# Performance work log

Hardware: AMD Instinct MI355X
Metric: run time of the kernel (lower is better)

## Reference

```python
import jax, jax.numpy as jnp
import numpy as np

EPS = 1e-6
LAM = 0.005


def setup_inputs() -> dict:
    key = jax.random.key(0)
    k1, k2, k3 = jax.random.split(key, 3)
    B, D, H, W, M = 16, 256, 128, 128, 4096
    z = jax.random.normal(k1, (B, D, H, W), dtype=jnp.float32)
    z_prime = jax.random.normal(k2, (B, D, H, W), dtype=jnp.float32)
    # Precomputed sampled pixel indices (flat over H*W). With randn inputs every
    # pixel passes the validity mask, so uniform sampling matches the original.
    flat_idx = jax.random.randint(k3, (B, M), 0, H * W, dtype=jnp.int32)
    return {"z": z, "z_prime": z_prime, "flat_idx": flat_idx}


def _gather_pixels(z, flat_idx):
    # z: (B, D, H, W), flat_idx: (B, M) -> (B*M, D)
    B, D, H, W = z.shape
    M = flat_idx.shape[1]
    z_flat = z.reshape(B, D, H * W)
    g = jnp.take_along_axis(z_flat, flat_idx[:, None, :], axis=2)  # (B, D, M)
    return g.transpose(0, 2, 1).reshape(B * M, D)


def _normalise(x):
    mean = jnp.mean(x, axis=0, keepdims=True)
    std = jnp.std(x, axis=0, keepdims=True, ddof=1)  # torch .std() is unbiased
    return (x - mean) / jnp.clip(std, EPS, None)


def reference(z, z_prime, flat_idx):
    D = z.shape[1]
    zm = _normalise(_gather_pixels(z, flat_idx))        # (N, D)
    zpm = _normalise(_gather_pixels(z_prime, flat_idx))  # (N, D)
    N = zm.shape[0]
    C = (zm.T @ zpm) / N                                 # (D, D)
    on_diag = jnp.diagonal(C)
    off_diag = C.reshape(-1)[1:].reshape(D - 1, D + 1)[:, :-1]
    loss = jnp.sum((1.0 - on_diag) ** 2) + LAM * jnp.sum(off_diag ** 2)
    return loss
```

## Files before the change

kernel.cpp:

```cpp
#include <hip/hip_runtime.h>
#include <hip/hip_bf16.h>

typedef short s16x8 __attribute__((ext_vector_type(8)));
typedef float f32x16 __attribute__((ext_vector_type(16)));

namespace {
constexpr int kB = 16;
constexpr int kD = 256;
constexpr int kHW = 16384;
constexpr int kM = 4096;
constexpr int kN = kB * kM;
constexpr int kWin = 1024;
constexpr int kNBlk = kB * (kHW / kWin);
constexpr int kKT = 32;
constexpr int kNIter = kWin / kKT;
constexpr float kLam = 0.005f;

__device__ __forceinline__ unsigned short f2bf(float f) {
    union { float f; unsigned u; } x{f};
    const unsigned r = x.u + 0x7FFFu + ((x.u >> 16) & 1u);
    return (unsigned short)(r >> 16);
}
}

__global__ __launch_bounds__(256) void count_kernel(
    const int* __restrict__ flat_idx, int* __restrict__ cnt)
{
    __shared__ int h[kHW];
    const int t = threadIdx.x;
    const int b = blockIdx.x;
    for (int i = t; i < kHW; i += 256) h[i] = 0;
    __syncthreads();
    const int* bi = flat_idx + b * kM;
    for (int i = t; i < kM; i += 256) atomicAdd(&h[bi[i]], 1);
    __syncthreads();
    int* dst = cnt + b * kHW;
    for (int i = t; i < kHW; i += 256) dst[i] = h[i];
}

__global__ __launch_bounds__(512, 2) void fused_gram_kernel(
    const float* __restrict__ z, const float* __restrict__ zp,
    const int* __restrict__ cnt,
    float* __restrict__ partial, float* __restrict__ statsPart)
{
    __shared__ char smem[65536];

    const int bx = blockIdx.x;
    const int b = bx & (kB - 1);
    const int win0 = (bx >> 4) * kWin;
    const int t = threadIdx.x;
    const int w = t >> 6, lane = t & 63, l31 = lane & 31, half = lane >> 5;
    const int wr = w >> 2;
    const int wc = w & 3;
    const int rbase = t >> 3;
    const int cg = t & 7;

    const float* zb  = z  + (size_t)b * kD * kHW;
    const float* zpb = zp + (size_t)b * kD * kHW;
    const int* cb = cnt + b * kHW;

    f32x16 acc[4][2];
#pragma unroll
    for (int i = 0; i < 4; ++i)
#pragma unroll
        for (int j = 0; j < 2; ++j)
#pragma unroll
            for (int r = 0; r < 16; ++r) acc[i][j][r] = 0.f;

    float sA[4], ssA[4], sB[4], ssB[4];
#pragma unroll
    for (int q = 0; q < 4; ++q) { sA[q] = ssA[q] = sB[q] = ssB[q] = 0.f; }

    float4 va[4], vb[4];
    int4 ci;

    auto LOAD = [&](int kt) {
        const int base = win0 + kt * kKT + cg * 4;
#pragma unroll
        for (int q = 0; q < 4; ++q) {
            const int row = 64 * q + rbase;
            va[q] = *(const float4*)(zb  + (size_t)row * kHW + base);
            vb[q] = *(const float4*)(zpb + (size_t)row * kHW + base);
        }
        ci = *(const int4*)(cb + base);
    };

    auto CONVERT = [&](int buf) {
        char* As = smem + buf * 32768;
        char* Bs = As + 16384;
        const float cf[4] = {(float)ci.x, (float)ci.y, (float)ci.z, (float)ci.w};
#pragma unroll
        for (int q = 0; q < 4; ++q) {
            const int row = 64 * q + rbase;
            const float a[4]  = {va[q].x, va[q].y, va[q].z, va[q].w};
            const float bb[4] = {vb[q].x, vb[q].y, vb[q].z, vb[q].w};
            ushort4 pa, pb;
            unsigned short* pav = (unsigned short*)&pa;
            unsigned short* pbv = (unsigned short*)&pb;
#pragma unroll
            for (int j = 0; j < 4; ++j) {
                const float wa = cf[j] * a[j];
                const float wb = cf[j] * bb[j];
                sA[q] += wa; ssA[q] += wa * a[j];
                sB[q] += wb; ssB[q] += wb * bb[j];
                pav[j] = f2bf(a[j]);
                pbv[j] = f2bf(wb);
            }
            const int off = row * 64 + (((cg >> 1) ^ ((row >> 1) & 3)) << 4)
                          + ((cg & 1) << 3);
            *(ushort4*)(As + off) = pa;
            *(ushort4*)(Bs + off) = pb;
        }
    };

    LOAD(0);
    CONVERT(0);
    LOAD(1);
    __syncthreads();

    for (int kt = 0; kt < kNIter; ++kt) {
        const char* As = smem + (kt & 1) * 32768;
        const char* Bs = As + 16384;
#pragma unroll
        for (int ks = 0; ks < 2; ++ks) {
            s16x8 af[4], bfr[2];
#pragma unroll
            for (int rt = 0; rt < 4; ++rt) {
                const int row = 128 * wr + 32 * rt + l31;
                const int o = (2 * ks + half) ^ ((row >> 1) & 3);
                af[rt] = *(const s16x8*)(As + row * 64 + o * 16);
            }
#pragma unroll
            for (int ct = 0; ct < 2; ++ct) {
                const int row = 64 * wc + 32 * ct + l31;
                const int o = (2 * ks + half) ^ ((row >> 1) & 3);
                bfr[ct] = *(const s16x8*)(Bs + row * 64 + o * 16);
            }
#pragma unroll
            for (int rt = 0; rt < 4; ++rt)
#pragma unroll
                for (int ct = 0; ct < 2; ++ct)
                    acc[rt][ct] = __builtin_amdgcn_mfma_f32_32x32x16_bf16(
                        af[rt], bfr[ct], acc[rt][ct], 0, 0, 0);
        }
        __syncthreads();
        if (kt < kNIter - 1) {
            CONVERT((kt + 1) & 1);
            if (kt < kNIter - 2) LOAD(kt + 2);
        }
        __syncthreads();
    }

    float* out = partial + (size_t)bx * (kD * kD);
#pragma unroll
    for (int rt = 0; rt < 4; ++rt)
#pragma unroll
        for (int ct = 0; ct < 2; ++ct)
#pragma unroll
            for (int r = 0; r < 16; ++r) {
                const int row = 128 * wr + 32 * rt + (r & 3) + 8 * (r >> 2) + 4 * half;
                const int col = 64 * wc + 32 * ct + l31;
                out[row * kD + col] = acc[rt][ct][r];
            }

    float* sd = (float*)smem;
#pragma unroll
    for (int q = 0; q < 4; ++q) {
        const int row = 64 * q + rbase;
        float* p = sd + (row * 8 + cg) * 4;
        p[0] = sA[q]; p[1] = ssA[q]; p[2] = sB[q]; p[3] = ssB[q];
    }
    __syncthreads();
    {
        const int row = t >> 1;
        const int pair = t & 1;
        float a0 = 0.f, a1 = 0.f;
#pragma unroll
        for (int g = 0; g < 8; ++g) {
            a0 += sd[(row * 8 + g) * 4 + 2 * pair];
            a1 += sd[(row * 8 + g) * 4 + 2 * pair + 1];
        }
        float* p = statsPart + ((size_t)bx * kD + row) * 4;
        p[2 * pair] = a0;
        p[2 * pair + 1] = a1;
    }
}

__global__ __launch_bounds__(256) void reduce_gram_kernel(
    const float* __restrict__ partial, float* __restrict__ G)
{
    const int d = blockIdx.x;
    const int e = threadIdx.x;
    float s = 0.f;
#pragma unroll 8
    for (int c = 0; c < kNBlk; ++c)
        s += partial[(size_t)c * (kD * kD) + d * kD + e];
    G[d * kD + e] = s;
}

__global__ __launch_bounds__(256) void loss_kernel(
    const float* __restrict__ G, const float* __restrict__ statsPart,
    float* __restrict__ out)
{
    __shared__ float muA[kD], isA[kD], muB[kD], isB[kD];
    const int t = threadIdx.x;
    float sA = 0.f, ssA = 0.f, sB = 0.f, ssB = 0.f;
    for (int blk = 0; blk < kNBlk; ++blk) {
        const float4 v = *(const float4*)(statsPart + ((size_t)blk * kD + t) * 4);
        sA += v.x; ssA += v.y; sB += v.z; ssB += v.w;
    }
    const float n = (float)kN;
    const float mA = sA / n, mB = sB / n;
    const float vA = (ssA - n * mA * mA) / (n - 1.f);
    const float vB = (ssB - n * mB * mB) / (n - 1.f);
    const float sdA = fmaxf(sqrtf(fmaxf(vA, 0.f)), 1e-6f);
    const float sdB = fmaxf(sqrtf(fmaxf(vB, 0.f)), 1e-6f);
    muA[t] = mA; isA[t] = 1.f / sdA;
    muB[t] = mB; isB[t] = 1.f / sdB;
    __syncthreads();

    float acc = 0.f;
    for (int d = 0; d < kD; ++d) {
        const int e = t;
        const float c = (G[d * kD + e] / n - muA[d] * muB[e]) * isA[d] * isB[e];
        if (d == e) { const float u = 1.f - c; acc += u * u; }
        else        { acc += kLam * c * c; }
    }
#pragma unroll
    for (int o = 32; o; o >>= 1) acc += __shfl_down(acc, o);
    __shared__ float r[4];
    if ((t & 63) == 0) r[t >> 6] = acc;
    __syncthreads();
    if (t == 0) out[0] = r[0] + r[1] + r[2] + r[3];
}

extern "C" void kernel_launch(void* const* d_in, const int* in_sizes, int n_in,
                              void* d_out, int out_size, void* d_ws, size_t ws_size,
                              hipStream_t stream) {
    const float* z  = (const float*)d_in[0];
    const float* zp = (const float*)d_in[1];
    const int* flat_idx = (const int*)d_in[2];
    float* out = (float*)d_out;

    char* ws = (char*)d_ws;
    int* cnt = (int*)ws;
    float* statsPart = (float*)(ws + (size_t)1 * 1024 * 1024);
    float* G = (float*)(ws + (size_t)2 * 1024 * 1024);
    float* partial = (float*)(ws + (size_t)16 * 1024 * 1024);

    count_kernel<<<kB, 256, 0, stream>>>(flat_idx, cnt);
    fused_gram_kernel<<<kNBlk, 512, 0, stream>>>(z, zp, cnt, partial, statsPart);
    reduce_gram_kernel<<<kD, 256, 0, stream>>>(partial, G);
    loss_kernel<<<1, 256, 0, stream>>>(G, statsPart, out);
}
```

Measured before the change: 182.1 us.

## Deepen gram-kernel prefetch to two register sets and parallelise stats reduction

The gram kernel now keeps two register sets of prefetched inputs, so global loads run two k-tiles ahead and the bf16 conversion of the next tile is issued before the MFMA step of the current one. The per-row statistics accumulation is rewritten as fma chains. The per-block statistics reduction, previously a serial 256-block loop inside the single-block loss kernel, moves into the reduce_gram kernel as a wave-shuffle reduction spread over all 256 blocks. The extra prefetch set raises register pressure under the 512x2 launch bound and could cause spills.

```diff
diff --git a/kernel.cpp b/kernel.cpp
--- a/kernel.cpp
+++ b/kernel.cpp
@@ -71,55 +71,56 @@
 #pragma unroll
     for (int q = 0; q < 4; ++q) { sA[q] = ssA[q] = sB[q] = ssB[q] = 0.f; }
 
-    float4 va[4], vb[4];
-    int4 ci;
-
-    auto LOAD = [&](int kt) {
-        const int base = win0 + kt * kKT + cg * 4;
-#pragma unroll
-        for (int q = 0; q < 4; ++q) {
-            const int row = 64 * q + rbase;
-            va[q] = *(const float4*)(zb  + (size_t)row * kHW + base);
-            vb[q] = *(const float4*)(zpb + (size_t)row * kHW + base);
-        }
-        ci = *(const int4*)(cb + base);
-    };
-
-    auto CONVERT = [&](int buf) {
-        char* As = smem + buf * 32768;
-        char* Bs = As + 16384;
-        const float cf[4] = {(float)ci.x, (float)ci.y, (float)ci.z, (float)ci.w};
-#pragma unroll
-        for (int q = 0; q < 4; ++q) {
-            const int row = 64 * q + rbase;
-            const float a[4]  = {va[q].x, va[q].y, va[q].z, va[q].w};
-            const float bb[4] = {vb[q].x, vb[q].y, vb[q].z, vb[q].w};
-            ushort4 pa, pb;
-            unsigned short* pav = (unsigned short*)&pa;
-            unsigned short* pbv = (unsigned short*)&pb;
-#pragma unroll
-            for (int j = 0; j < 4; ++j) {
-                const float wa = cf[j] * a[j];
-                const float wb = cf[j] * bb[j];
-                sA[q] += wa; ssA[q] += wa * a[j];
-                sB[q] += wb; ssB[q] += wb * bb[j];
-                pav[j] = f2bf(a[j]);
-                pbv[j] = f2bf(wb);
-            }
-            const int off = row * 64 + (((cg >> 1) ^ ((row >> 1) & 3)) << 4)
-                          + ((cg & 1) << 3);
-            *(ushort4*)(As + off) = pa;
-            *(ushort4*)(Bs + off) = pb;
-        }
-    };
-
-    LOAD(0);
-    CONVERT(0);
-    LOAD(1);
-    __syncthreads();
-
-    for (int kt = 0; kt < kNIter; ++kt) {
-        const char* As = smem + (kt & 1) * 32768;
+    float4 va0[4], vb0[4], va1[4], vb1[4];
+    int4 ci0, ci1;
+
+#define LOAD_SET(S, kt)                                                     \
+    {                                                                       \
+        const int base_ = win0 + (kt) * kKT + cg * 4;                       \
+        _Pragma("unroll")                                                   \
+        for (int q = 0; q < 4; ++q) {                                       \
+            const int row_ = 64 * q + rbase;                                \
+            va##S[q] = *(const float4*)(zb  + (size_t)row_ * kHW + base_);  \
+            vb##S[q] = *(const float4*)(zpb + (size_t)row_ * kHW + base_);  \
+        }                                                                   \
+        ci##S = *(const int4*)(cb + base_);                                 \
+    }
+
+#define CONV_SET(S, buf)                                                    \
+    {                                                                       \
+        char* As_ = smem + (buf) * 32768;                                   \
+        char* Bs_ = As_ + 16384;                                            \
+        const float cf_[4] = {(float)ci##S.x, (float)ci##S.y,               \
+                              (float)ci##S.z, (float)ci##S.w};              \
+        _Pragma("unroll")                                                   \
+        for (int q = 0; q < 4; ++q) {                                       \
+            const int row_ = 64 * q + rbase;                                \
+            const float a_[4]  = {va##S[q].x, va##S[q].y, va##S[q].z, va##S[q].w}; \
+            const float bb_[4] = {vb##S[q].x, vb##S[q].y, vb##S[q].z, vb##S[q].w}; \
+            ushort4 pa_, pb_;                                               \
+            unsigned short* pav_ = (unsigned short*)&pa_;                   \
+            unsigned short* pbv_ = (unsigned short*)&pb_;                   \
+            _Pragma("unroll")                                               \
+            for (int j = 0; j < 4; ++j) {                                   \
+                const float a2_ = a_[j] * a_[j];                            \
+                const float b2_ = bb_[j] * bb_[j];                          \
+                const float wb_ = cf_[j] * bb_[j];                          \
+                sA[q] = fmaf(cf_[j], a_[j], sA[q]);                         \
+                ssA[q] = fmaf(cf_[j], a2_, ssA[q]);                         \
+                sB[q] = fmaf(cf_[j], bb_[j], sB[q]);                        \
+                ssB[q] = fmaf(cf_[j], b2_, ssB[q]);                         \
+                pav_[j] = f2bf(a_[j]);                                      \
+                pbv_[j] = f2bf(wb_);                                        \
+            }                                                               \
+            const int off_ = row_ * 64 + (((cg >> 1) ^ ((row_ >> 1) & 3)) << 4) \
+                           + ((cg & 1) << 3);                               \
+            *(ushort4*)(As_ + off_) = pa_;                                  \
+            *(ushort4*)(Bs_ + off_) = pb_;                                  \
+        }                                                                   \
+    }
+
+    auto MFMA_STEP = [&](int buf) {
+        const char* As = smem + buf * 32768;
         const char* Bs = As + 16384;
 #pragma unroll
         for (int ks = 0; ks < 2; ++ks) {
@@ -143,11 +144,23 @@
                     acc[rt][ct] = __builtin_amdgcn_mfma_f32_32x32x16_bf16(
                         af[rt], bfr[ct], acc[rt][ct], 0, 0, 0);
         }
+    };
+
+    LOAD_SET(0, 0)
+    CONV_SET(0, 0)
+    LOAD_SET(1, 1)
+    LOAD_SET(0, 2)
+    __syncthreads();
+
+    for (int kt = 0; kt < kNIter; kt += 2) {
+        CONV_SET(1, 1)
+        if (kt + 3 < kNIter) LOAD_SET(1, kt + 3)
+        MFMA_STEP(0);
         __syncthreads();
-        if (kt < kNIter - 1) {
-            CONVERT((kt + 1) & 1);
-            if (kt < kNIter - 2) LOAD(kt + 2);
-        }
+
+        if (kt + 2 < kNIter) CONV_SET(0, 0)
+        if (kt + 4 < kNIter) LOAD_SET(0, kt + 4)
+        MFMA_STEP(1);
         __syncthreads();
     }
 
@@ -184,10 +197,13 @@
         p[2 * pair] = a0;
         p[2 * pair + 1] = a1;
     }
+#undef LOAD_SET
+#undef CONV_SET
 }
 
 __global__ __launch_bounds__(256) void reduce_gram_kernel(
-    const float* __restrict__ partial, float* __restrict__ G)
+    const float* __restrict__ partial, const float* __restrict__ statsPart,
+    float* __restrict__ G, float* __restrict__ statsRed)
 {
     const int d = blockIdx.x;
     const int e = threadIdx.x;
@@ -196,23 +212,38 @@
     for (int c = 0; c < kNBlk; ++c)
         s += partial[(size_t)c * (kD * kD) + d * kD + e];
     G[d * kD + e] = s;
+
+    const float4 v = *(const float4*)(statsPart + ((size_t)e * kD + d) * 4);
+    float x0 = v.x, x1 = v.y, x2 = v.z, x3 = v.w;
+#pragma unroll
+    for (int o = 32; o; o >>= 1) {
+        x0 += __shfl_down(x0, o);
+        x1 += __shfl_down(x1, o);
+        x2 += __shfl_down(x2, o);
+        x3 += __shfl_down(x3, o);
+    }
+    __shared__ float r[4][4];
+    if ((e & 63) == 0) {
+        r[e >> 6][0] = x0; r[e >> 6][1] = x1;
+        r[e >> 6][2] = x2; r[e >> 6][3] = x3;
+    }
+    __syncthreads();
+    if (e < 4) {
+        statsRed[d * 4 + e] = r[0][e] + r[1][e] + r[2][e] + r[3][e];
+    }
 }
 
 __global__ __launch_bounds__(256) void loss_kernel(
-    const float* __restrict__ G, const float* __restrict__ statsPart,
+    const float* __restrict__ G, const float* __restrict__ statsRed,
     float* __restrict__ out)
 {
     __shared__ float muA[kD], isA[kD], muB[kD], isB[kD];
     const int t = threadIdx.x;
-    float sA = 0.f, ssA = 0.f, sB = 0.f, ssB = 0.f;
-    for (int blk = 0; blk < kNBlk; ++blk) {
-        const float4 v = *(const float4*)(statsPart + ((size_t)blk * kD + t) * 4);
-        sA += v.x; ssA += v.y; sB += v.z; ssB += v.w;
-    }
+    const float4 v = *(const float4*)(statsRed + t * 4);
     const float n = (float)kN;
-    const float mA = sA / n, mB = sB / n;
-    const float vA = (ssA - n * mA * mA) / (n - 1.f);
-    const float vB = (ssB - n * mB * mB) / (n - 1.f);
+    const float mA = v.x / n, mB = v.z / n;
+    const float vA = (v.y - n * mA * mA) / (n - 1.f);
+    const float vB = (v.w - n * mB * mB) / (n - 1.f);
     const float sdA = fmaxf(sqrtf(fmaxf(vA, 0.f)), 1e-6f);
     const float sdB = fmaxf(sqrtf(fmaxf(vB, 0.f)), 1e-6f);
     muA[t] = mA; isA[t] = 1.f / sdA;
@@ -245,11 +276,12 @@
     char* ws = (char*)d_ws;
     int* cnt = (int*)ws;
     float* statsPart = (float*)(ws + (size_t)1 * 1024 * 1024);
-    float* G = (float*)(ws + (size_t)2 * 1024 * 1024);
+    float* statsRed  = (float*)(ws + (size_t)2 * 1024 * 1024);
+    float* G = (float*)(ws + (size_t)2 * 1024 * 1024 + 64 * 1024);
     float* partial = (float*)(ws + (size_t)16 * 1024 * 1024);
 
     count_kernel<<<kB, 256, 0, stream>>>(flat_idx, cnt);
     fused_gram_kernel<<<kNBlk, 512, 0, stream>>>(z, zp, cnt, partial, statsPart);
-    reduce_gram_kernel<<<kD, 256, 0, stream>>>(partial, G);
-    loss_kernel<<<1, 256, 0, stream>>>(G, statsPart, out);
-}
+    reduce_gram_kernel<<<kD, 256, 0, stream>>>(partial, statsPart, G, statsRed);
+    loss_kernel<<<1, 256, 0, stream>>>(G, statsRed, out);
+}
```

After: 270.3 us. 1.48x slower.
